# Optimization experiments

Hardware: AMD Instinct MI355X
Metric: run time of the kernel (lower is better)

The kernel has to match this reference:

```python
import jax, jax.numpy as jnp
import numpy as np

VOCAB = 96
HIDDEN = 128
DEPTH = 500          # total ReLU iterations per character (num_layers=1)
BPTT_DEPTH = 20      # only affects backward (truncated BPTT)
EPS = 1e-6


def _rms_norm(x, scale):
    # x: (B, H). RMSNorm: x / sqrt(mean(x^2) + eps) * scale
    rms = jnp.sqrt(jnp.mean(x * x, axis=-1, keepdims=True) + EPS)
    return x / rms * scale


def setup_inputs() -> dict:
    key = jax.random.key(0)
    ks = jax.random.split(key, 6)
    B, S = 64, 32
    chars = jax.random.randint(ks[0], (B, S), 0, VOCAB)
    hidden = jnp.zeros((B, HIDDEN), dtype=jnp.float32)
    # embedding ~ N(0, 0.02)
    embed_w = 0.02 * jax.random.normal(ks[1], (VOCAB, HIDDEN), dtype=jnp.float32)
    # orthogonal recurrent weight, scaled by 1/sqrt(num_layers)=1 (num_layers=1)
    W = jnp.linalg.qr(jax.random.normal(ks[2], (HIDDEN, HIDDEN), dtype=jnp.float32))[0]
    b = jnp.zeros((HIDDEN,), dtype=jnp.float32)
    pre_scale = jnp.ones((HIDDEN,), dtype=jnp.float32)
    post_scale = jnp.ones((HIDDEN,), dtype=jnp.float32)
    # readout: xavier-uniform (VOCAB, HIDDEN), zero bias
    limit = float(np.sqrt(6.0 / (VOCAB + HIDDEN)))
    readout_w = jax.random.uniform(ks[3], (VOCAB, HIDDEN), dtype=jnp.float32,
                                   minval=-limit, maxval=limit)
    readout_b = jnp.zeros((VOCAB,), dtype=jnp.float32)
    return {"chars": chars, "hidden": hidden, "embed_w": embed_w, "W": W,
            "b": b, "pre_scale": pre_scale, "post_scale": post_scale,
            "readout_w": readout_w, "readout_b": readout_b}


def reference(chars, hidden, embed_w, W, b, pre_scale, post_scale,
              readout_w, readout_b):
    # chars: (B, S) int; hidden: (B, H)
    embeds = embed_w[chars]                       # (B, S, H)

    def recur_step(h, _):
        # h = h + relu(RMSNorm(h) @ W + e + b), e closed over per timestep
        return h, None

    def time_step(h, e):
        # DEPTH sequential residual-ReLU iterations with embed injection
        def step(hc, _):
            hc = hc + jax.nn.relu(_rms_norm(hc, pre_scale) @ W + e + b)
            return hc, None
        h, _ = jax.lax.scan(step, h, None, length=DEPTH)
        h = _rms_norm(h, post_scale)              # hidden is replaced by post_norm
        logits = h @ readout_w.T + readout_b      # (B, V)
        return h, logits

    h_final, logits = jax.lax.scan(time_step, hidden,
                                   jnp.swapaxes(embeds, 0, 1))  # scan over S
    logits = jnp.swapaxes(logits, 0, 1)           # (B, S, V)
    return logits, jax.lax.stop_gradient(h_final)
```

## Files before the change

### kernel.cpp

```cpp
#include <hip/hip_runtime.h>

#define BSZ 64
#define SLEN 32
#define HID 128
#define VOC 96
#define DEPTH 500
#define TPB 256
#define EPSV 1e-6f
#define PAD 20

typedef __attribute__((ext_vector_type(2))) float f32x2;

#if defined(__has_builtin)
#if __has_builtin(__builtin_elementwise_fma)
#define VFMA(a, b, c) __builtin_elementwise_fma((a), (b), (c))
#endif
#endif
#ifndef VFMA
__device__ __forceinline__ f32x2 vfma_(f32x2 a, f32x2 b, f32x2 c) {
    f32x2 r; r.x = fmaf(a.x, b.x, c.x); r.y = fmaf(a.y, b.y, c.y); return r;
}
#define VFMA(a, b, c) vfma_((a), (b), (c))
#endif

__device__ __forceinline__ float rsq_fast(float x) {
    float r; asm("v_rsq_f32 %0, %1" : "=v"(r) : "v"(x)); return r;
}

template <int CTRL>
__device__ __forceinline__ float qperm(float v) {
    return __int_as_float(__builtin_amdgcn_update_dpp(
        0, __float_as_int(v), CTRL, 0xF, 0xF, true));
}
#define BFLY8(v)                                                               \
    v += qperm<0xB1>(v);                                             \
    v += qperm<0x4E>(v);                                             \
    v += __int_as_float(__builtin_amdgcn_ds_swizzle(__float_as_int(v), 0x101F));

__global__ __launch_bounds__(TPB, 1) void rnn_char_lm(
    const int* __restrict__ chars, const float* __restrict__ hidden,
    const float* __restrict__ embed_w, const float* __restrict__ W_g,
    const float* __restrict__ b_g, const float* __restrict__ pre_s,
    const float* __restrict__ post_s, const float* __restrict__ rw_g,
    const float* __restrict__ rb_g, float* __restrict__ out)
{
    __shared__ __align__(16) float hbuf[2][8 * PAD];
    __shared__ float rwT[HID * VOC];

    const int b = blockIdx.x;
    const int tid = threadIdx.x;
    const int w = tid >> 6;
    const int lane = tid & 63;
    const int g = lane >> 3;
    const int ch = lane & 7;

    const int col0 = 32 * w + 4 * g;
    const int widx = PAD * (col0 >> 4) + (col0 & 15);
    const int rbase = PAD * ch;

    for (int e = tid; e < VOC * HID; e += TPB) {
        int v = e >> 7;
        int k = e & (HID - 1);
        rwT[k * VOC + v] = rw_g[e];
    }

    f32x2 W2[4][8];
#pragma unroll
    for (int q = 0; q < 8; ++q) {
        int k0 = 16 * ch + 2 * q;
        float p0 = pre_s[k0], p1 = pre_s[k0 + 1];
#pragma unroll
        for (int c = 0; c < 4; ++c) {
            f32x2 t;
            t.x = p0 * W_g[k0 * HID + col0 + c];
            t.y = p1 * W_g[(k0 + 1) * HID + col0 + c];
            W2[c][q] = t;
        }
    }
    const float4 bv  = *(const float4*)&b_g[col0];
    const float4 psv = *(const float4*)&post_s[col0];
    const float rbv = (tid < VOC) ? rb_g[tid] : 0.0f;

    float4 hc = *(const float4*)&hidden[b * HID + col0];

    if (ch == 0) *(float4*)&hbuf[0][widx] = hc;
    __syncthreads();

#define ITER(P)                                                                \
    {                                                                          \
        const float4* rb = (const float4*)&hbuf[P][rbase];                     \
        float4 x0 = rb[0], x1 = rb[1], x2 = rb[2], x3 = rb[3];                 \
        f32x2 a0 = {0,0}, a1 = {0,0}, a2 = {0,0}, a3 = {0,0}, s = {0,0};       \
        _Pragma("unroll")                                                      \
        for (int q = 0; q < 8; ++q) {                                          \
            const float4 xq = (q < 2) ? x0 : (q < 4) ? x1 : (q < 6) ? x2 : x3; \
            f32x2 hv;                                                          \
            hv.x = (q & 1) ? xq.z : xq.x;                                      \
            hv.y = (q & 1) ? xq.w : xq.y;                                      \
            s  = VFMA(hv, hv, s);                                              \
            a0 = VFMA(hv, W2[0][q], a0);                                       \
            a1 = VFMA(hv, W2[1][q], a1);                                       \
            a2 = VFMA(hv, W2[2][q], a2);                                       \
            a3 = VFMA(hv, W2[3][q], a3);                                       \
        }                                                                      \
        float y0 = a0.x + a0.y, y1 = a1.x + a1.y;                              \
        float y2 = a2.x + a2.y, y3 = a3.x + a3.y;                              \
        float ssl = s.x + s.y;                                                 \
        BFLY8(y0) BFLY8(y1) BFLY8(y2) BFLY8(y3) BFLY8(ssl)                     \
        const float rn = rsq_fast(fmaf(ssl, 1.0f / HID, EPSV));                \
        hc.x += fmaxf(fmaf(y0, rn, ev.x), 0.0f);                               \
        hc.y += fmaxf(fmaf(y1, rn, ev.y), 0.0f);                               \
        hc.z += fmaxf(fmaf(y2, rn, ev.z), 0.0f);                               \
        hc.w += fmaxf(fmaf(y3, rn, ev.w), 0.0f);                               \
        if (ch == 0) *(float4*)&hbuf[P ^ 1][widx] = hc;                        \
        __syncthreads();                                                       \
    }

    for (int t = 0; t < SLEN; ++t) {
        const int c = chars[b * SLEN + t];
        const float4 er = *(const float4*)&embed_w[c * HID + col0];
        float4 ev;
        ev.x = er.x + bv.x; ev.y = er.y + bv.y;
        ev.z = er.z + bv.z; ev.w = er.w + bv.w;

        for (int it = 0; it < DEPTH / 2; ++it) {
            ITER(0)
            ITER(1)
        }

        {
            const float4* rb = (const float4*)&hbuf[0][rbase];
            float4 x0 = rb[0], x1 = rb[1], x2 = rb[2], x3 = rb[3];
            f32x2 s = {0, 0};
            f32x2 hv;
            hv.x = x0.x; hv.y = x0.y; s = VFMA(hv, hv, s);
            hv.x = x0.z; hv.y = x0.w; s = VFMA(hv, hv, s);
            hv.x = x1.x; hv.y = x1.y; s = VFMA(hv, hv, s);
            hv.x = x1.z; hv.y = x1.w; s = VFMA(hv, hv, s);
            hv.x = x2.x; hv.y = x2.y; s = VFMA(hv, hv, s);
            hv.x = x2.z; hv.y = x2.w; s = VFMA(hv, hv, s);
            hv.x = x3.x; hv.y = x3.y; s = VFMA(hv, hv, s);
            hv.x = x3.z; hv.y = x3.w; s = VFMA(hv, hv, s);
            float ssl = s.x + s.y;
            BFLY8(ssl)
            const float rnp = 1.0f / sqrtf(ssl * (1.0f / HID) + EPSV);
            hc.x *= rnp * psv.x; hc.y *= rnp * psv.y;
            hc.z *= rnp * psv.z; hc.w *= rnp * psv.w;
            __syncthreads();
            if (ch == 0) *(float4*)&hbuf[0][widx] = hc;
            __syncthreads();
        }

        if (tid < VOC) {
            float acc0 = 0.0f, acc1 = 0.0f;
#pragma unroll
            for (int C = 0; C < 8; ++C) {
#pragma unroll
                for (int m4 = 0; m4 < 4; ++m4) {
                    const float4 x = *(const float4*)&hbuf[0][PAD * C + 4 * m4];
                    const int k = 16 * C + 4 * m4;
                    acc0 = fmaf(x.x, rwT[(k + 0) * VOC + tid], acc0);
                    acc1 = fmaf(x.y, rwT[(k + 1) * VOC + tid], acc1);
                    acc0 = fmaf(x.z, rwT[(k + 2) * VOC + tid], acc0);
                    acc1 = fmaf(x.w, rwT[(k + 3) * VOC + tid], acc1);
                }
            }
            out[(b * SLEN + t) * VOC + tid] = acc0 + acc1 + rbv;
        }
    }

    if (ch == 0)
        *(float4*)&out[BSZ * SLEN * VOC + b * HID + col0] = hc;

#undef ITER
}

extern "C" void kernel_launch(void* const* d_in, const int* in_sizes, int n_in,
                              void* d_out, int out_size, void* d_ws, size_t ws_size,
                              hipStream_t stream)
{
    const int* chars      = (const int*)d_in[0];
    const float* hidden   = (const float*)d_in[1];
    const float* embed_w  = (const float*)d_in[2];
    const float* W_g      = (const float*)d_in[3];
    const float* b_g      = (const float*)d_in[4];
    const float* pre_s    = (const float*)d_in[5];
    const float* post_s   = (const float*)d_in[6];
    const float* rw_g     = (const float*)d_in[7];
    const float* rb_g     = (const float*)d_in[8];
    float* out            = (float*)d_out;

    rnn_char_lm<<<dim3(BSZ), dim3(TPB), 0, stream>>>(
        chars, hidden, embed_w, W_g, b_g, pre_s, post_s, rw_g, rb_g, out);
}
```

Measured before the change: 4.480 ms.

## Halve block to two waves with four-lane K split per column group

Reduces the block from 256 to 128 threads so each lane holds a 32-row slice of W for four columns, and the per-column dot-product reduction runs over 4 lanes using only DPP instead of 8 lanes with a ds_swizzle. The shared-memory layout of the hidden state changes to 4 chunks of 36 floats. The aim is to shorten the latency-bound serial iteration: the barrier spans fewer waves and the cross-lane reduction has fewer steps. In exchange, each lane does twice the FMAs per iteration and holds twice as many weight registers.

```diff
diff --git a/kernel.cpp b/kernel.cpp
--- a/kernel.cpp
+++ b/kernel.cpp
@@ -5,9 +5,9 @@
 #define HID 128
 #define VOC 96
 #define DEPTH 500
-#define TPB 256
+#define TPB 128
 #define EPSV 1e-6f
-#define PAD 20
+#define CHK 36
 
 typedef __attribute__((ext_vector_type(2))) float f32x2;
 
@@ -32,10 +32,9 @@
     return __int_as_float(__builtin_amdgcn_update_dpp(
         0, __float_as_int(v), CTRL, 0xF, 0xF, true));
 }
-#define BFLY8(v)                                                               \
+#define BFLY4(v)                                                               \
     v += qperm<0xB1>(v);                                             \
-    v += qperm<0x4E>(v);                                             \
-    v += __int_as_float(__builtin_amdgcn_ds_swizzle(__float_as_int(v), 0x101F));
+    v += qperm<0x4E>(v);
 
 __global__ __launch_bounds__(TPB, 1) void rnn_char_lm(
     const int* __restrict__ chars, const float* __restrict__ hidden,
@@ -44,19 +43,19 @@
     const float* __restrict__ post_s, const float* __restrict__ rw_g,
     const float* __restrict__ rb_g, float* __restrict__ out)
 {
-    __shared__ __align__(16) float hbuf[2][8 * PAD];
+    __shared__ __align__(16) float hbuf[2][4 * CHK];
     __shared__ float rwT[HID * VOC];
 
     const int b = blockIdx.x;
     const int tid = threadIdx.x;
-    const int w = tid >> 6;
+    const int wv = tid >> 6;
     const int lane = tid & 63;
-    const int g = lane >> 3;
-    const int ch = lane & 7;
+    const int g = lane >> 2;
+    const int ch = lane & 3;
 
-    const int col0 = 32 * w + 4 * g;
-    const int widx = PAD * (col0 >> 4) + (col0 & 15);
-    const int rbase = PAD * ch;
+    const int col0 = 64 * wv + 4 * g;
+    const int widx = CHK * (col0 >> 5) + (col0 & 31);
+    const int rbase = CHK * ch;
 
     for (int e = tid; e < VOC * HID; e += TPB) {
         int v = e >> 7;
@@ -64,10 +63,10 @@
         rwT[k * VOC + v] = rw_g[e];
     }
 
-    f32x2 W2[4][8];
+    f32x2 W2[4][16];
 #pragma unroll
-    for (int q = 0; q < 8; ++q) {
-        int k0 = 16 * ch + 2 * q;
+    for (int q = 0; q < 16; ++q) {
+        int k0 = 32 * ch + 2 * q;
         float p0 = pre_s[k0], p1 = pre_s[k0 + 1];
 #pragma unroll
         for (int c = 0; c < 4; ++c) {
@@ -90,10 +89,13 @@
     {                                                                          \
         const float4* rb = (const float4*)&hbuf[P][rbase];                     \
         float4 x0 = rb[0], x1 = rb[1], x2 = rb[2], x3 = rb[3];                 \
+        float4 x4 = rb[4], x5 = rb[5], x6 = rb[6], x7 = rb[7];                 \
         f32x2 a0 = {0,0}, a1 = {0,0}, a2 = {0,0}, a3 = {0,0}, s = {0,0};       \
         _Pragma("unroll")                                                      \
-        for (int q = 0; q < 8; ++q) {                                          \
-            const float4 xq = (q < 2) ? x0 : (q < 4) ? x1 : (q < 6) ? x2 : x3; \
+        for (int q = 0; q < 16; ++q) {                                         \
+            const float4 xq = (q < 2) ? x0 : (q < 4) ? x1 : (q < 6) ? x2 :     \
+                              (q < 8) ? x3 : (q < 10) ? x4 : (q < 12) ? x5 :   \
+                              (q < 14) ? x6 : x7;                              \
             f32x2 hv;                                                          \
             hv.x = (q & 1) ? xq.z : xq.x;                                      \
             hv.y = (q & 1) ? xq.w : xq.y;                                      \
@@ -106,7 +108,7 @@
         float y0 = a0.x + a0.y, y1 = a1.x + a1.y;                              \
         float y2 = a2.x + a2.y, y3 = a3.x + a3.y;                              \
         float ssl = s.x + s.y;                                                 \
-        BFLY8(y0) BFLY8(y1) BFLY8(y2) BFLY8(y3) BFLY8(ssl)                     \
+        BFLY4(y0) BFLY4(y1) BFLY4(y2) BFLY4(y3) BFLY4(ssl)                     \
         const float rn = rsq_fast(fmaf(ssl, 1.0f / HID, EPSV));                \
         hc.x += fmaxf(fmaf(y0, rn, ev.x), 0.0f);                               \
         hc.y += fmaxf(fmaf(y1, rn, ev.y), 0.0f);                               \
@@ -130,19 +132,16 @@
 
         {
             const float4* rb = (const float4*)&hbuf[0][rbase];
-            float4 x0 = rb[0], x1 = rb[1], x2 = rb[2], x3 = rb[3];
             f32x2 s = {0, 0};
-            f32x2 hv;
-            hv.x = x0.x; hv.y = x0.y; s = VFMA(hv, hv, s);
-            hv.x = x0.z; hv.y = x0.w; s = VFMA(hv, hv, s);
-            hv.x = x1.x; hv.y = x1.y; s = VFMA(hv, hv, s);
-            hv.x = x1.z; hv.y = x1.w; s = VFMA(hv, hv, s);
-            hv.x = x2.x; hv.y = x2.y; s = VFMA(hv, hv, s);
-            hv.x = x2.z; hv.y = x2.w; s = VFMA(hv, hv, s);
-            hv.x = x3.x; hv.y = x3.y; s = VFMA(hv, hv, s);
-            hv.x = x3.z; hv.y = x3.w; s = VFMA(hv, hv, s);
+#pragma unroll
+            for (int q8 = 0; q8 < 8; ++q8) {
+                float4 x = rb[q8];
+                f32x2 hv;
+                hv.x = x.x; hv.y = x.y; s = VFMA(hv, hv, s);
+                hv.x = x.z; hv.y = x.w; s = VFMA(hv, hv, s);
+            }
             float ssl = s.x + s.y;
-            BFLY8(ssl)
+            BFLY4(ssl)
             const float rnp = 1.0f / sqrtf(ssl * (1.0f / HID) + EPSV);
             hc.x *= rnp * psv.x; hc.y *= rnp * psv.y;
             hc.z *= rnp * psv.z; hc.w *= rnp * psv.w;
@@ -154,11 +153,11 @@
         if (tid < VOC) {
             float acc0 = 0.0f, acc1 = 0.0f;
 #pragma unroll
-            for (int C = 0; C < 8; ++C) {
+            for (int C = 0; C < 4; ++C) {
 #pragma unroll
-                for (int m4 = 0; m4 < 4; ++m4) {
-                    const float4 x = *(const float4*)&hbuf[0][PAD * C + 4 * m4];
-                    const int k = 16 * C + 4 * m4;
+                for (int m4 = 0; m4 < 8; ++m4) {
+                    const float4 x = *(const float4*)&hbuf[0][CHK * C + 4 * m4];
+                    const int k = 32 * C + 4 * m4;
                     acc0 = fmaf(x.x, rwT[(k + 0) * VOC + tid], acc0);
                     acc1 = fmaf(x.y, rwT[(k + 1) * VOC + tid], acc1);
                     acc0 = fmaf(x.z, rwT[(k + 2) * VOC + tid], acc0);
```

Result: slower. 4.969 ms (+10.9%).
